# Kernel tuning notes

Measured on AMD Instinct MI355X. Metric: run time of the kernel, lower is better.

The kernel has to match this reference:

```python
import jax, jax.numpy as jnp
import numpy as np

D_K = 128  # query/key dim, used for the 1/sqrt(d_k) scale


def setup_inputs() -> dict:
    key = jax.random.key(0)
    k1, k2, k3, k4 = jax.random.split(key, 4)
    B, L, d_model, d_k, d_v = 4, 2048, 1024, 128, 128

    def xavier(k, shape):
        # matches nn.init.xavier_uniform_ for 2D weights
        limit = np.sqrt(6.0 / (shape[0] + shape[1]))
        return jax.random.uniform(k, shape, jnp.float32, -limit, limit)

    return {
        "X": jax.random.normal(k1, (B, L, d_model), jnp.float32),
        "W_Q": xavier(k2, (d_model, d_k)),
        "W_K": xavier(k3, (d_model, d_k)),
        "W_V": xavier(k4, (d_model, d_v)),
    }


def reference(X, W_Q, W_K, W_V):
    # X: (B, L, d_model)
    L = X.shape[1]
    Q = jnp.einsum("bld,dk->blk", X, W_Q)          # (B, L, d_k)
    K = jnp.einsum("bld,dk->blk", X, W_K)          # (B, L, d_k)
    V = jnp.einsum("bld,dv->blv", X, W_V)          # (B, L, d_v)
    scale = D_K ** -0.5
    scores = jnp.einsum("bqk,bpk->bqp", Q, K) * scale  # (B, L, L)
    # causal mask: positions above the diagonal set to -inf
    causal = jnp.tril(jnp.ones((L, L), dtype=bool))
    scores = jnp.where(causal, scores, -jnp.inf)
    A = jax.nn.softmax(scores, axis=-1)            # (B, L, L)
    Z = jnp.einsum("bqp,bpv->bqv", A, V)           # (B, L, d_v)
    return Z
```

## Files before the change

kernel.cpp:

```cpp
#include <hip/hip_runtime.h>
#include <hip/hip_bf16.h>

typedef __bf16 bf16;
typedef __attribute__((ext_vector_type(4))) __bf16 bf16x4;
typedef __attribute__((ext_vector_type(8))) __bf16 bf16x8;
typedef __attribute__((ext_vector_type(4))) float f32x4;

#define D_MODEL 1024
#define DK 128
#define LSEQ 2048
#define NQT 128
#define NB 4
#define SCALE2 (0.08838834764831845f * 1.4426950408889634f)

__global__ __launch_bounds__(256) void wt_kernel(
    const float* __restrict__ Wq, const float* __restrict__ Wk,
    const float* __restrict__ Wv, bf16* __restrict__ Wt)
{
    __shared__ bf16 tile[64][72];
    const float* W = (blockIdx.z == 0) ? Wq : (blockIdx.z == 1) ? Wk : Wv;
    int k0 = blockIdx.x * 64;
    int n0 = blockIdx.y * 64;
    int t  = threadIdx.x;
    #pragma unroll
    for (int i = 0; i < 16; ++i) {
        int idx = t + i * 256;
        int r = idx >> 6, c = idx & 63;
        tile[c][r] = (bf16)W[(size_t)(k0 + r) * DK + n0 + c];
    }
    __syncthreads();
    bf16* out = Wt + (size_t)blockIdx.z * DK * D_MODEL;
    #pragma unroll
    for (int i = 0; i < 16; ++i) {
        int idx = t + i * 256;
        int rr = idx >> 6, cc = idx & 63;
        out[(size_t)(n0 + rr) * D_MODEL + k0 + cc] = tile[rr][cc];
    }
}

__global__ __launch_bounds__(256) void proj_kernel(
    const float* __restrict__ X, const bf16* __restrict__ Wt,
    bf16* __restrict__ Qs, bf16* __restrict__ Kb, bf16* __restrict__ Vt)
{
    __shared__ bf16 Xs[64][72];
    __shared__ bf16 Ws[128][72];
    int mt = blockIdx.x, mat = blockIdx.y;
    const bf16* W = Wt + (size_t)mat * DK * D_MODEL;
    int t = threadIdx.x;
    int wave = t >> 6, lane = t & 63;
    int lq = lane & 15, g = lane >> 4;
    int row0 = mt * 64;

    f32x4 acc[4][2];
    #pragma unroll
    for (int m = 0; m < 4; ++m)
        #pragma unroll
        for (int n = 0; n < 2; ++n) acc[m][n] = f32x4{0.f, 0.f, 0.f, 0.f};

    f32x4  rxf[4];
    bf16x8 rw[4];
    auto LOADR = [&](int k0) {
        #pragma unroll
        for (int i = 0; i < 4; ++i) {
            int u = t + i * 256, r = u >> 4, c4 = u & 15;
            rxf[i] = *reinterpret_cast<const f32x4*>(
                &X[(size_t)(row0 + r) * D_MODEL + k0 + c4 * 4]);
        }
        #pragma unroll
        for (int i = 0; i < 4; ++i) {
            int u = t + i * 256, r = u >> 3, c8 = u & 7;
            rw[i] = *reinterpret_cast<const bf16x8*>(
                &W[(size_t)r * D_MODEL + k0 + c8 * 8]);
        }
    };
    auto STORER = [&]() {
        #pragma unroll
        for (int i = 0; i < 4; ++i) {
            int u = t + i * 256, r = u >> 4, c4 = u & 15;
            bf16x4 h;
            h[0]=(bf16)rxf[i][0]; h[1]=(bf16)rxf[i][1];
            h[2]=(bf16)rxf[i][2]; h[3]=(bf16)rxf[i][3];
            *reinterpret_cast<bf16x4*>(&Xs[r][c4 * 4]) = h;
        }
        #pragma unroll
        for (int i = 0; i < 4; ++i) {
            int u = t + i * 256, r = u >> 3, c8 = u & 7;
            *reinterpret_cast<bf16x8*>(&Ws[r][c8 * 8]) = rw[i];
        }
    };

    LOADR(0);
    for (int ks = 0; ks < 16; ++ks) {
        __syncthreads();
        STORER();
        if (ks + 1 < 16) LOADR((ks + 1) * 64);
        __syncthreads();
        #pragma unroll
        for (int kk = 0; kk < 2; ++kk) {
            bf16x8 a[4];
            #pragma unroll
            for (int mr = 0; mr < 4; ++mr)
                a[mr] = *reinterpret_cast<const bf16x8*>(&Xs[mr * 16 + lq][kk * 32 + g * 8]);
            #pragma unroll
            for (int n = 0; n < 2; ++n) {
                bf16x8 bfr = *reinterpret_cast<const bf16x8*>(
                    &Ws[wave * 32 + n * 16 + lq][kk * 32 + g * 8]);
                #pragma unroll
                for (int mr = 0; mr < 4; ++mr)
                    acc[mr][n] = __builtin_amdgcn_mfma_f32_16x16x32_bf16(a[mr], bfr, acc[mr][n], 0, 0, 0);
            }
        }
    }
    #pragma unroll
    for (int mr = 0; mr < 4; ++mr) {
        int orow = row0 + mr * 16 + g * 4;
        #pragma unroll
        for (int n = 0; n < 2; ++n) {
            int col = wave * 32 + n * 16 + lq;
            if (mat == 0) {
                #pragma unroll
                for (int r = 0; r < 4; ++r)
                    Qs[(size_t)(orow + r) * DK + col] = (bf16)(acc[mr][n][r] * SCALE2);
            } else if (mat == 1) {
                #pragma unroll
                for (int r = 0; r < 4; ++r)
                    Kb[(size_t)(orow + r) * DK + col] = (bf16)acc[mr][n][r];
            } else {
                int bb  = orow >> 11;
                int kv0 = orow & 2047;
                bf16x4 h;
                h[0]=(bf16)acc[mr][n][0]; h[1]=(bf16)acc[mr][n][1];
                h[2]=(bf16)acc[mr][n][2]; h[3]=(bf16)acc[mr][n][3];
                *reinterpret_cast<bf16x4*>(
                    &Vt[((size_t)bb * DK + col) * LSEQ + kv0]) = h;
            }
        }
    }
}

__global__ __launch_bounds__(256, 3) void attn_kernel(
    const bf16* __restrict__ Qs, const bf16* __restrict__ Kb,
    const bf16* __restrict__ Vt, bf16* __restrict__ Zp,
    float* __restrict__ Mp, float* __restrict__ Lp,
    float* __restrict__ Out, int split)
{
    __shared__ bf16 Ks[64][136];
    __shared__ bf16 Vs[128][72];
    __shared__ bf16 P[4][16][72];
    int bid = blockIdx.x;
    int b, qblk, s;
    if (split) {
        int xcd = bid & 7, u = bid >> 3;
        b = xcd >> 1;
        int n2 = (u << 1) | (xcd & 1);
        int q = 0, off = 0;
        while (off + ((q >> 2) + 1) <= n2) { off += (q >> 2) + 1; ++q; }
        qblk = q;
        s = n2 - off;
    } else {
        b = bid >> 5;
        qblk = bid & 31;
        s = 0;
    }
    int t = threadIdx.x;
    int wave = t >> 6, lane = t & 63;
    int lq = lane & 15, g = lane >> 4;
    int qw16 = qblk * 4 + wave;
    int qg = qw16 * 16 + lq;

    int nt = qblk + 1;
    int t0 = split ? 4 * s : 0;
    int t1 = split ? min(4 * s + 4, nt) : nt;

    const bf16* Kbase = Kb + (size_t)b * LSEQ * DK;
    const bf16* Vbase = Vt + (size_t)b * DK * LSEQ;

    const bf16* Qrow = Qs + ((size_t)b * LSEQ + qg) * DK;
    bf16x8 qf[4];
    #pragma unroll
    for (int ks = 0; ks < 4; ++ks)
        qf[ks] = *reinterpret_cast<const bf16x8*>(&Qrow[ks * 32 + g * 8]);

    f32x4 z[8];
    #pragma unroll
    for (int i = 0; i < 8; ++i) z[i] = f32x4{0.f, 0.f, 0.f, 0.f};
    float mrun = -3.0e38f, lrun = 0.f;

    bf16x8 kreg[4], vreg[4];
    auto LOADKV = [&](int kvb) {
        #pragma unroll
        for (int i = 0; i < 4; ++i) {
            int u = t + i * 256, r = u >> 4, c = u & 15;
            kreg[i] = *reinterpret_cast<const bf16x8*>(
                &Kbase[(size_t)(kvb + r) * DK + c * 8]);
        }
        #pragma unroll
        for (int i = 0; i < 4; ++i) {
            int u = t + i * 256, d = u >> 3, c = u & 7;
            vreg[i] = *reinterpret_cast<const bf16x8*>(
                &Vbase[(size_t)d * LSEQ + kvb + c * 8]);
        }
    };
    auto STOREKV = [&]() {
        #pragma unroll
        for (int i = 0; i < 4; ++i) {
            int u = t + i * 256, r = u >> 4, c = u & 15;
            *reinterpret_cast<bf16x8*>(&Ks[r][c * 8]) = kreg[i];
        }
        #pragma unroll
        for (int i = 0; i < 4; ++i) {
            int u = t + i * 256, d = u >> 3, c = u & 7;
            *reinterpret_cast<bf16x8*>(&Vs[d][c * 8]) = vreg[i];
        }
    };

    LOADKV(t0 * 64);
    for (int ti = t0; ti < t1; ++ti) {
        int kvb = ti * 64;
        __syncthreads();
        STOREKV();
        if (ti + 1 < t1) LOADKV((ti + 1) * 64);
        __syncthreads();

        f32x4 sc[4];
        #pragma unroll
        for (int jj = 0; jj < 4; ++jj) sc[jj] = f32x4{0.f, 0.f, 0.f, 0.f};
        __builtin_amdgcn_s_setprio(1);
        #pragma unroll
        for (int jj = 0; jj < 4; ++jj)
            #pragma unroll
            for (int ks = 0; ks < 4; ++ks) {
                bf16x8 a = *reinterpret_cast<const bf16x8*>(
                    &Ks[jj * 16 + lq][ks * 32 + g * 8]);
                sc[jj] = __builtin_amdgcn_mfma_f32_16x16x32_bf16(a, qf[ks], sc[jj], 0, 0, 0);
            }
        __builtin_amdgcn_s_setprio(0);

        float sv[16];
        if (ti == nt - 1) {
            #pragma unroll
            for (int jj = 0; jj < 4; ++jj)
                #pragma unroll
                for (int r = 0; r < 4; ++r) {
                    int kv0 = kvb + jj * 16 + g * 4 + r;
                    sv[jj * 4 + r] = (kv0 <= qg) ? sc[jj][r] : -3.0e38f;
                }
        } else {
            #pragma unroll
            for (int jj = 0; jj < 4; ++jj)
                #pragma unroll
                for (int r = 0; r < 4; ++r) sv[jj * 4 + r] = sc[jj][r];
        }
        float mt = sv[0];
        #pragma unroll
        for (int i = 1; i < 16; ++i) mt = fmaxf(mt, sv[i]);
        mt = fmaxf(mt, __shfl_xor(mt, 16));
        mt = fmaxf(mt, __shfl_xor(mt, 32));
        if (!__all(mt <= mrun)) {
            float mnew  = fmaxf(mrun, mt);
            float alpha = exp2f(mrun - mnew);
            lrun *= alpha;
            #pragma unroll
            for (int i = 0; i < 8; ++i) {
                z[i][0] *= alpha; z[i][1] *= alpha; z[i][2] *= alpha; z[i][3] *= alpha;
            }
            mrun = mnew;
        }
        float psum = 0.f;
        #pragma unroll
        for (int jj = 0; jj < 4; ++jj) {
            bf16x4 pb;
            #pragma unroll
            for (int r = 0; r < 4; ++r) {
                float e = exp2f(sv[jj * 4 + r] - mrun);
                psum += e;
                pb[r] = (bf16)e;
            }
            *reinterpret_cast<bf16x4*>(&P[wave][lq][jj * 16 + g * 4]) = pb;
        }
        psum += __shfl_xor(psum, 16);
        psum += __shfl_xor(psum, 32);
        lrun += psum;
        __builtin_amdgcn_s_setprio(1);
        #pragma unroll
        for (int sl = 0; sl < 2; ++sl) {
            bf16x8 pf = *reinterpret_cast<const bf16x8*>(&P[wave][lq][sl * 32 + g * 8]);
            #pragma unroll
            for (int dt = 0; dt < 8; ++dt) {
                bf16x8 av = *reinterpret_cast<const bf16x8*>(
                    &Vs[dt * 16 + lq][sl * 32 + g * 8]);
                z[dt] = __builtin_amdgcn_mfma_f32_16x16x32_bf16(av, pf, z[dt], 0, 0, 0);
            }
        }
        __builtin_amdgcn_s_setprio(0);
    }

    int S = (qblk >> 2) + 1;
    if (!split || S == 1) {
        float inv = 1.f / lrun;
        float* orow = Out + ((size_t)b * LSEQ + qg) * DK;
        #pragma unroll
        for (int dt = 0; dt < 8; ++dt) {
            f32x4 v;
            v[0]=z[dt][0]*inv; v[1]=z[dt][1]*inv; v[2]=z[dt][2]*inv; v[3]=z[dt][3]*inv;
            *reinterpret_cast<f32x4*>(&orow[dt * 16 + g * 4]) = v;
        }
    } else {
        size_t T = ((size_t)(b * NQT + qw16) * 8 + s);
        bf16* zp = Zp + T * (16 * 128);
        #pragma unroll
        for (int dt = 0; dt < 8; ++dt) {
            bf16x4 h;
            h[0]=(bf16)z[dt][0]; h[1]=(bf16)z[dt][1];
            h[2]=(bf16)z[dt][2]; h[3]=(bf16)z[dt][3];
            *reinterpret_cast<bf16x4*>(&zp[lq * 128 + dt * 16 + g * 4]) = h;
        }
        if (g == 0) {
            Mp[T * 16 + lq] = mrun;
            Lp[T * 16 + lq] = lrun;
        }
    }
}

__global__ __launch_bounds__(256) void combine_kernel(
    const bf16* __restrict__ Zp, const float* __restrict__ Mp,
    const float* __restrict__ Lp, float* __restrict__ Out)
{
    int qt = blockIdx.x + 16, b = blockIdx.y;
    int S  = (qt >> 4) + 1;
    int t  = threadIdx.x;
    int r  = t >> 4;
    int d0 = (t & 15) * 8;
    size_t Tbase = (size_t)(b * NQT + qt) * 8;

    float m = -3.0e38f;
    for (int s = 0; s < S; ++s)
        m = fmaxf(m, Mp[(Tbase + s) * 16 + r]);

    float L = 0.f;
    float a[8] = {0.f, 0.f, 0.f, 0.f, 0.f, 0.f, 0.f, 0.f};
    for (int s = 0; s < S; ++s) {
        float w = exp2f(Mp[(Tbase + s) * 16 + r] - m);
        L += w * Lp[(Tbase + s) * 16 + r];
        bf16x8 v = *reinterpret_cast<const bf16x8*>(
            &Zp[(Tbase + s) * (16 * 128) + r * 128 + d0]);
        #pragma unroll
        for (int j = 0; j < 8; ++j) a[j] += w * (float)v[j];
    }
    float inv = 1.f / L;
    float* orow = Out + ((size_t)b * LSEQ + qt * 16 + r) * DK + d0;
    f32x4 o0, o1;
    o0[0]=a[0]*inv; o0[1]=a[1]*inv; o0[2]=a[2]*inv; o0[3]=a[3]*inv;
    o1[0]=a[4]*inv; o1[1]=a[5]*inv; o1[2]=a[6]*inv; o1[3]=a[7]*inv;
    *reinterpret_cast<f32x4*>(&orow[0]) = o0;
    *reinterpret_cast<f32x4*>(&orow[4]) = o1;
}

extern "C" void kernel_launch(void* const* d_in, const int* in_sizes, int n_in,
                              void* d_out, int out_size, void* d_ws, size_t ws_size,
                              hipStream_t stream)
{
    const float* X  = (const float*)d_in[0];
    const float* Wq = (const float*)d_in[1];
    const float* Wk = (const float*)d_in[2];
    const float* Wv = (const float*)d_in[3];
    float* Out = (float*)d_out;

    char* ws = (char*)d_ws;
    bf16* Wt = (bf16*)(ws);
    bf16* Qs = (bf16*)(ws + ((size_t)1 << 20));
    bf16* Kb = (bf16*)(ws + ((size_t)3 << 20));
    bf16* Vt = (bf16*)(ws + ((size_t)5 << 20));
    size_t base = (size_t)7 << 20;

    size_t zp_bytes = (size_t)NB * NQT * 8 * 16 * 128 * 2;
    size_t ml_bytes = (size_t)NB * NQT * 8 * 16 * 4;
    int split = (ws_size >= base + zp_bytes + 2 * ml_bytes) ? 1 : 0;

    bf16*  Zp = (bf16*)(ws + base);
    float* Mp = (float*)(ws + base + zp_bytes);
    float* Lp = (float*)(ws + base + zp_bytes + ml_bytes);

    hipLaunchKernelGGL(wt_kernel,   dim3(16, 2, 3), dim3(256), 0, stream, Wq, Wk, Wv, Wt);
    hipLaunchKernelGGL(proj_kernel, dim3(128, 3),   dim3(256), 0, stream, X, Wt, Qs, Kb, Vt);
    hipLaunchKernelGGL(attn_kernel, dim3(split ? 576 : NB * 32), dim3(256), 0, stream,
                       Qs, Kb, Vt, Zp, Mp, Lp, Out, split);
    if (split)
        hipLaunchKernelGGL(combine_kernel, dim3(112, NB), dim3(256), 0, stream,
                           Zp, Mp, Lp, Out);
}
```

Measured before the change: 50.77 us.

## Use direct global-to-LDS loads, XOR-swizzled K/V layout, and two query tiles per wave

The projection kernel now writes K and V^T with an XOR swizzle on 16-byte chunks. This lets the attention kernel copy them straight into unpadded LDS using global_load_lds, avoiding the register round-trip and bank conflicts. Attention blocks drop to 128 threads (2 waves), and each wave processes two 16-row query tiles, so every K/V fragment read from LDS feeds two MFMAs. In exchange, the register prefetch of the next KV tile is gone (staging is now synchronous between barriers), and register pressure per wave roughly doubles.

```diff
diff --git a/kernel.cpp b/kernel.cpp
--- a/kernel.cpp
+++ b/kernel.cpp
@@ -12,6 +12,10 @@
 #define NQT 128
 #define NB 4
 #define SCALE2 (0.08838834764831845f * 1.4426950408889634f)
+
+#define GLD16(g, l) __builtin_amdgcn_global_load_lds(                       \
+    (const __attribute__((address_space(1))) void*)(g),                     \
+    (__attribute__((address_space(3))) void*)(l), 16, 0, 0)
 
 __global__ __launch_bounds__(256) void wt_kernel(
     const float* __restrict__ Wq, const float* __restrict__ Wk,
@@ -122,31 +126,37 @@
                 for (int r = 0; r < 4; ++r)
                     Qs[(size_t)(orow + r) * DK + col] = (bf16)(acc[mr][n][r] * SCALE2);
             } else if (mat == 1) {
+                int colg = col >> 3, cre = col & 7;
                 #pragma unroll
-                for (int r = 0; r < 4; ++r)
-                    Kb[(size_t)(orow + r) * DK + col] = (bf16)acc[mr][n][r];
+                for (int r = 0; r < 4; ++r) {
+                    int row = orow + r;
+                    Kb[(size_t)row * DK + ((colg ^ (row & 7)) << 3) + cre]
+                        = (bf16)acc[mr][n][r];
+                }
             } else {
                 int bb  = orow >> 11;
                 int kv0 = orow & 2047;
+                int gv  = ((kv0 & 63) >> 3) ^ (col & 7);
                 bf16x4 h;
                 h[0]=(bf16)acc[mr][n][0]; h[1]=(bf16)acc[mr][n][1];
                 h[2]=(bf16)acc[mr][n][2]; h[3]=(bf16)acc[mr][n][3];
                 *reinterpret_cast<bf16x4*>(
-                    &Vt[((size_t)bb * DK + col) * LSEQ + kv0]) = h;
+                    &Vt[((size_t)bb * DK + col) * LSEQ + (kv0 & ~63) + (gv << 3) + (kv0 & 7)]) = h;
             }
         }
     }
 }
 
-__global__ __launch_bounds__(256, 3) void attn_kernel(
+__global__ __launch_bounds__(128, 2) void attn_kernel(
     const bf16* __restrict__ Qs, const bf16* __restrict__ Kb,
     const bf16* __restrict__ Vt, bf16* __restrict__ Zp,
     float* __restrict__ Mp, float* __restrict__ Lp,
     float* __restrict__ Out, int split)
 {
-    __shared__ bf16 Ks[64][136];
-    __shared__ bf16 Vs[128][72];
-    __shared__ bf16 P[4][16][72];
+    __shared__ __align__(16) bf16 Ks[64][128];
+    __shared__ __align__(16) bf16 Vs[128][64];
+    __shared__ bf16 P[2][32][72];
+
     int bid = blockIdx.x;
     int b, qblk, s;
     if (split) {
@@ -165,8 +175,9 @@
     int t = threadIdx.x;
     int wave = t >> 6, lane = t & 63;
     int lq = lane & 15, g = lane >> 4;
-    int qw16 = qblk * 4 + wave;
-    int qg = qw16 * 16 + lq;
+    int key = lq & 7;
+    int qg0 = qblk * 64 + wave * 32 + lq;
+    int qg1 = qg0 + 16;
 
     int nt = qblk + 1;
     int t0 = split ? 4 * s : 0;
@@ -175,121 +186,143 @@
     const bf16* Kbase = Kb + (size_t)b * LSEQ * DK;
     const bf16* Vbase = Vt + (size_t)b * DK * LSEQ;
 
-    const bf16* Qrow = Qs + ((size_t)b * LSEQ + qg) * DK;
-    bf16x8 qf[4];
-    #pragma unroll
-    for (int ks = 0; ks < 4; ++ks)
-        qf[ks] = *reinterpret_cast<const bf16x8*>(&Qrow[ks * 32 + g * 8]);
-
-    f32x4 z[8];
-    #pragma unroll
-    for (int i = 0; i < 8; ++i) z[i] = f32x4{0.f, 0.f, 0.f, 0.f};
-    float mrun = -3.0e38f, lrun = 0.f;
-
-    bf16x8 kreg[4], vreg[4];
-    auto LOADKV = [&](int kvb) {
-        #pragma unroll
-        for (int i = 0; i < 4; ++i) {
-            int u = t + i * 256, r = u >> 4, c = u & 15;
-            kreg[i] = *reinterpret_cast<const bf16x8*>(
-                &Kbase[(size_t)(kvb + r) * DK + c * 8]);
-        }
-        #pragma unroll
-        for (int i = 0; i < 4; ++i) {
-            int u = t + i * 256, d = u >> 3, c = u & 7;
-            vreg[i] = *reinterpret_cast<const bf16x8*>(
-                &Vbase[(size_t)d * LSEQ + kvb + c * 8]);
-        }
+    const bf16* Qrow0 = Qs + ((size_t)b * LSEQ + qg0) * DK;
+    bf16x8 qf0[4], qf1[4];
+    #pragma unroll
+    for (int ks = 0; ks < 4; ++ks) {
+        qf0[ks] = *reinterpret_cast<const bf16x8*>(&Qrow0[ks * 32 + g * 8]);
+        qf1[ks] = *reinterpret_cast<const bf16x8*>(&Qrow0[16 * DK + ks * 32 + g * 8]);
+    }
+
+    f32x4 z0[8], z1[8];
+    #pragma unroll
+    for (int i = 0; i < 8; ++i) {
+        z0[i] = f32x4{0.f, 0.f, 0.f, 0.f};
+        z1[i] = f32x4{0.f, 0.f, 0.f, 0.f};
+    }
+    float mrun0 = -3.0e38f, lrun0 = 0.f;
+    float mrun1 = -3.0e38f, lrun1 = 0.f;
+
+    auto STAGE = [&](int kvb) {
+        const char* kg = (const char*)(Kbase + (size_t)kvb * DK) + (size_t)t * 16;
+        char* kl = (char*)(&Ks[0][0]) + (size_t)t * 16;
+        #pragma unroll
+        for (int i = 0; i < 8; ++i)
+            GLD16(kg + i * 2048, kl + i * 2048);
+        const char* vg = (const char*)Vbase + (size_t)(t >> 3) * (LSEQ * 2)
+                       + (size_t)kvb * 2 + (t & 7) * 16;
+        char* vl = (char*)(&Vs[0][0]) + (size_t)t * 16;
+        #pragma unroll
+        for (int i = 0; i < 8; ++i)
+            GLD16(vg + (size_t)i * 16 * (LSEQ * 2), vl + i * 2048);
     };
-    auto STOREKV = [&]() {
-        #pragma unroll
-        for (int i = 0; i < 4; ++i) {
-            int u = t + i * 256, r = u >> 4, c = u & 15;
-            *reinterpret_cast<bf16x8*>(&Ks[r][c * 8]) = kreg[i];
-        }
-        #pragma unroll
-        for (int i = 0; i < 4; ++i) {
-            int u = t + i * 256, d = u >> 3, c = u & 7;
-            *reinterpret_cast<bf16x8*>(&Vs[d][c * 8]) = vreg[i];
-        }
-    };
-
-    LOADKV(t0 * 64);
+
     for (int ti = t0; ti < t1; ++ti) {
         int kvb = ti * 64;
         __syncthreads();
-        STOREKV();
-        if (ti + 1 < t1) LOADKV((ti + 1) * 64);
+        STAGE(kvb);
         __syncthreads();
 
-        f32x4 sc[4];
-        #pragma unroll
-        for (int jj = 0; jj < 4; ++jj) sc[jj] = f32x4{0.f, 0.f, 0.f, 0.f};
+        f32x4 sc0[4], sc1[4];
+        #pragma unroll
+        for (int jj = 0; jj < 4; ++jj) {
+            sc0[jj] = f32x4{0.f, 0.f, 0.f, 0.f};
+            sc1[jj] = f32x4{0.f, 0.f, 0.f, 0.f};
+        }
         __builtin_amdgcn_s_setprio(1);
         #pragma unroll
-        for (int jj = 0; jj < 4; ++jj)
+        for (int jj = 0; jj < 4; ++jj) {
+            const char* kr = (const char*)&Ks[jj * 16 + lq][0];
             #pragma unroll
             for (int ks = 0; ks < 4; ++ks) {
                 bf16x8 a = *reinterpret_cast<const bf16x8*>(
-                    &Ks[jj * 16 + lq][ks * 32 + g * 8]);
-                sc[jj] = __builtin_amdgcn_mfma_f32_16x16x32_bf16(a, qf[ks], sc[jj], 0, 0, 0);
-            }
+                    kr + (((4 * ks + g) ^ key) << 4));
+                sc0[jj] = __builtin_amdgcn_mfma_f32_16x16x32_bf16(a, qf0[ks], sc0[jj], 0, 0, 0);
+                sc1[jj] = __builtin_amdgcn_mfma_f32_16x16x32_bf16(a, qf1[ks], sc1[jj], 0, 0, 0);
+            }
+        }
         __builtin_amdgcn_s_setprio(0);
 
-        float sv[16];
+        float sv0[16], sv1[16];
         if (ti == nt - 1) {
             #pragma unroll
             for (int jj = 0; jj < 4; ++jj)
                 #pragma unroll
                 for (int r = 0; r < 4; ++r) {
                     int kv0 = kvb + jj * 16 + g * 4 + r;
-                    sv[jj * 4 + r] = (kv0 <= qg) ? sc[jj][r] : -3.0e38f;
+                    sv0[jj * 4 + r] = (kv0 <= qg0) ? sc0[jj][r] : -3.0e38f;
+                    sv1[jj * 4 + r] = (kv0 <= qg1) ? sc1[jj][r] : -3.0e38f;
                 }
         } else {
             #pragma unroll
             for (int jj = 0; jj < 4; ++jj)
                 #pragma unroll
-                for (int r = 0; r < 4; ++r) sv[jj * 4 + r] = sc[jj][r];
-        }
-        float mt = sv[0];
-        #pragma unroll
-        for (int i = 1; i < 16; ++i) mt = fmaxf(mt, sv[i]);
-        mt = fmaxf(mt, __shfl_xor(mt, 16));
-        mt = fmaxf(mt, __shfl_xor(mt, 32));
-        if (!__all(mt <= mrun)) {
-            float mnew  = fmaxf(mrun, mt);
-            float alpha = exp2f(mrun - mnew);
-            lrun *= alpha;
+                for (int r = 0; r < 4; ++r) {
+                    sv0[jj * 4 + r] = sc0[jj][r];
+                    sv1[jj * 4 + r] = sc1[jj][r];
+                }
+        }
+
+        float mt0 = sv0[0], mt1 = sv1[0];
+        #pragma unroll
+        for (int i = 1; i < 16; ++i) { mt0 = fmaxf(mt0, sv0[i]); mt1 = fmaxf(mt1, sv1[i]); }
+        mt0 = fmaxf(mt0, __shfl_xor(mt0, 16));
+        mt0 = fmaxf(mt0, __shfl_xor(mt0, 32));
+        mt1 = fmaxf(mt1, __shfl_xor(mt1, 16));
+        mt1 = fmaxf(mt1, __shfl_xor(mt1, 32));
+        if (!__all(mt0 <= mrun0)) {
+            float mnew  = fmaxf(mrun0, mt0);
+            float alpha = exp2f(mrun0 - mnew);
+            lrun0 *= alpha;
             #pragma unroll
             for (int i = 0; i < 8; ++i) {
-                z[i][0] *= alpha; z[i][1] *= alpha; z[i][2] *= alpha; z[i][3] *= alpha;
-            }
-            mrun = mnew;
-        }
-        float psum = 0.f;
+                z0[i][0] *= alpha; z0[i][1] *= alpha; z0[i][2] *= alpha; z0[i][3] *= alpha;
+            }
+            mrun0 = mnew;
+        }
+        if (!__all(mt1 <= mrun1)) {
+            float mnew  = fmaxf(mrun1, mt1);
+            float alpha = exp2f(mrun1 - mnew);
+            lrun1 *= alpha;
+            #pragma unroll
+            for (int i = 0; i < 8; ++i) {
+                z1[i][0] *= alpha; z1[i][1] *= alpha; z1[i][2] *= alpha; z1[i][3] *= alpha;
+            }
+            mrun1 = mnew;
+        }
+        float psum0 = 0.f, psum1 = 0.f;
         #pragma unroll
         for (int jj = 0; jj < 4; ++jj) {
-            bf16x4 pb;
+            bf16x4 pb0, pb1;
             #pragma unroll
             for (int r = 0; r < 4; ++r) {
-                float e = exp2f(sv[jj * 4 + r] - mrun);
-                psum += e;
-                pb[r] = (bf16)e;
-            }
-            *reinterpret_cast<bf16x4*>(&P[wave][lq][jj * 16 + g * 4]) = pb;
-        }
-        psum += __shfl_xor(psum, 16);
-        psum += __shfl_xor(psum, 32);
-        lrun += psum;
+                float e0 = exp2f(sv0[jj * 4 + r] - mrun0);
+                float e1 = exp2f(sv1[jj * 4 + r] - mrun1);
+                psum0 += e0; psum1 += e1;
+                pb0[r] = (bf16)e0; pb1[r] = (bf16)e1;
+            }
+            *reinterpret_cast<bf16x4*>(&P[wave][lq][jj * 16 + g * 4])      = pb0;
+            *reinterpret_cast<bf16x4*>(&P[wave][16 + lq][jj * 16 + g * 4]) = pb1;
+        }
+        psum0 += __shfl_xor(psum0, 16);
+        psum0 += __shfl_xor(psum0, 32);
+        psum1 += __shfl_xor(psum1, 16);
+        psum1 += __shfl_xor(psum1, 32);
+        lrun0 += psum0;
+        lrun1 += psum1;
+
         __builtin_amdgcn_s_setprio(1);
         #pragma unroll
         for (int sl = 0; sl < 2; ++sl) {
-            bf16x8 pf = *reinterpret_cast<const bf16x8*>(&P[wave][lq][sl * 32 + g * 8]);
+            bf16x8 pf0 = *reinterpret_cast<const bf16x8*>(&P[wave][lq][sl * 32 + g * 8]);
+            bf16x8 pf1 = *reinterpret_cast<const bf16x8*>(&P[wave][16 + lq][sl * 32 + g * 8]);
             #pragma unroll
             for (int dt = 0; dt < 8; ++dt) {
+                const char* vr = (const char*)&Vs[dt * 16 + lq][0];
                 bf16x8 av = *reinterpret_cast<const bf16x8*>(
-                    &Vs[dt * 16 + lq][sl * 32 + g * 8]);
-                z[dt] = __builtin_amdgcn_mfma_f32_16x16x32_bf16(av, pf, z[dt], 0, 0, 0);
+                    vr + (((4 * sl + g) ^ key) << 4));
+                z0[dt] = __builtin_amdgcn_mfma_f32_16x16x32_bf16(av, pf0, z0[dt], 0, 0, 0);
+                z1[dt] = __builtin_amdgcn_mfma_f32_16x16x32_bf16(av, pf1, z1[dt], 0, 0, 0);
             }
         }
         __builtin_amdgcn_s_setprio(0);
@@ -297,27 +330,36 @@
 
     int S = (qblk >> 2) + 1;
     if (!split || S == 1) {
-        float inv = 1.f / lrun;
-        float* orow = Out + ((size_t)b * LSEQ + qg) * DK;
+        float inv0 = 1.f / lrun0, inv1 = 1.f / lrun1;
+        float* o0 = Out + ((size_t)b * LSEQ + qg0) * DK;
+        float* o1 = Out + ((size_t)b * LSEQ + qg1) * DK;
         #pragma unroll
         for (int dt = 0; dt < 8; ++dt) {
-            f32x4 v;
-            v[0]=z[dt][0]*inv; v[1]=z[dt][1]*inv; v[2]=z[dt][2]*inv; v[3]=z[dt][3]*inv;
-            *reinterpret_cast<f32x4*>(&orow[dt * 16 + g * 4]) = v;
+            f32x4 v0, v1;
+            v0[0]=z0[dt][0]*inv0; v0[1]=z0[dt][1]*inv0; v0[2]=z0[dt][2]*inv0; v0[3]=z0[dt][3]*inv0;
+            v1[0]=z1[dt][0]*inv1; v1[1]=z1[dt][1]*inv1; v1[2]=z1[dt][2]*inv1; v1[3]=z1[dt][3]*inv1;
+            *reinterpret_cast<f32x4*>(&o0[dt * 16 + g * 4]) = v0;
+            *reinterpret_cast<f32x4*>(&o1[dt * 16 + g * 4]) = v1;
         }
     } else {
-        size_t T = ((size_t)(b * NQT + qw16) * 8 + s);
-        bf16* zp = Zp + T * (16 * 128);
+        int qw0 = qblk * 4 + wave * 2;
+        size_t T0 = ((size_t)(b * NQT + qw0)     * 8 + s);
+        size_t T1 = ((size_t)(b * NQT + qw0 + 1) * 8 + s);
+        bf16* zp0 = Zp + T0 * (16 * 128);
+        bf16* zp1 = Zp + T1 * (16 * 128);
         #pragma unroll
         for (int dt = 0; dt < 8; ++dt) {
-            bf16x4 h;
-            h[0]=(bf16)z[dt][0]; h[1]=(bf16)z[dt][1];
-            h[2]=(bf16)z[dt][2]; h[3]=(bf16)z[dt][3];
-            *reinterpret_cast<bf16x4*>(&zp[lq * 128 + dt * 16 + g * 4]) = h;
+            bf16x4 h0, h1;
+            h0[0]=(bf16)z0[dt][0]; h0[1]=(bf16)z0[dt][1]; h0[2]=(bf16)z0[dt][2]; h0[3]=(bf16)z0[dt][3];
+            h1[0]=(bf16)z1[dt][0]; h1[1]=(bf16)z1[dt][1]; h1[2]=(bf16)z1[dt][2]; h1[3]=(bf16)z1[dt][3];
+            *reinterpret_cast<bf16x4*>(&zp0[lq * 128 + dt * 16 + g * 4]) = h0;
+            *reinterpret_cast<bf16x4*>(&zp1[lq * 128 + dt * 16 + g * 4]) = h1;
         }
         if (g == 0) {
-            Mp[T * 16 + lq] = mrun;
-            Lp[T * 16 + lq] = lrun;
+            Mp[T0 * 16 + lq] = mrun0;
+            Lp[T0 * 16 + lq] = lrun0;
+            Mp[T1 * 16 + lq] = mrun1;
+            Lp[T1 * 16 + lq] = lrun1;
         }
     }
 }
@@ -383,7 +425,7 @@
 
     hipLaunchKernelGGL(wt_kernel,   dim3(16, 2, 3), dim3(256), 0, stream, Wq, Wk, Wv, Wt);
     hipLaunchKernelGGL(proj_kernel, dim3(128, 3),   dim3(256), 0, stream, X, Wt, Qs, Kb, Vt);
-    hipLaunchKernelGGL(attn_kernel, dim3(split ? 576 : NB * 32), dim3(256), 0, stream,
+    hipLaunchKernelGGL(attn_kernel, dim3(split ? 576 : NB * 32), dim3(128), 0, stream,
                        Qs, Kb, Vt, Zp, Mp, Lp, Out, split);
     if (split)
         hipLaunchKernelGGL(combine_kernel, dim3(112, NB), dim3(256), 0, stream,
```

Measured after the change: 53.74 us. 1.06x slower.
